# Performance work log

Measured on AMD Instinct MI355X. Metric: run time of the kernel, lower is better.

Reference implementation:

```python
import jax, jax.numpy as jnp
import numpy as np

N, E = 50000, 800000          # nodes, directed edges
DIN, DH, DOUT = 128, 256, 128  # feature dims


def setup_inputs() -> dict:
    key = jax.random.key(0)
    ks = jax.random.split(key, 8)
    glorot = lambda k, fin, fout: jax.random.normal(k, (fin, fout), jnp.float32) * np.float32(1.0 / np.sqrt(fin))
    x = jax.random.normal(ks[0], (N, DIN), jnp.float32)
    edge_index = jax.random.randint(ks[1], (2, E), 0, N, dtype=jnp.int64)
    return {
        "x": x,
        "edge_index": edge_index,
        "W1_l": glorot(ks[2], DIN, DH),   # applied to aggregated neighbors
        "b1": jnp.zeros((DH,), jnp.float32),
        "W1_r": glorot(ks[3], DIN, DH),   # root weight
        "W2_l": glorot(ks[4], DH, DOUT),
        "b2": jnp.zeros((DOUT,), jnp.float32),
        "W2_r": glorot(ks[5], DH, DOUT),
    }


def _sage_conv(x, src, dst, W_l, b, W_r):
    """PyG SAGEConv (mean aggr): lin_l(mean_j x_j) + lin_r(x_i)."""
    n = x.shape[0]
    agg = jax.ops.segment_sum(x[src], dst, num_segments=n)          # [N, D]
    deg = jax.ops.segment_sum(jnp.ones((src.shape[0], 1), x.dtype), dst, num_segments=n)
    agg = agg / jnp.maximum(deg, 1.0)                               # mean over in-neighbors
    return agg @ W_l + b + x @ W_r


def reference(x, edge_index, W1_l, b1, W1_r, W2_l, b2, W2_r):
    src, dst = edge_index[0], edge_index[1]
    h = jax.nn.relu(_sage_conv(x, src, dst, W1_l, b1, W1_r))
    return _sage_conv(h, src, dst, W2_l, b2, W2_r)
```

## Files before the change

kernel.cpp:

```cpp
#include <hip/hip_runtime.h>
#include <hip/hip_bf16.h>
#include <cstdint>


static inline size_t align_up(size_t x, size_t a) { return (x + a - 1) & ~(a - 1); }

using short8 = __attribute__((ext_vector_type(8))) short;
using f32x4  = __attribute__((ext_vector_type(4))) float;

#define BSHIFT 6
#define PB 98

__device__ __forceinline__ float bfpair_lo(unsigned int v) {
  union { unsigned int i; float f; } u; u.i = v << 16; return u.f;
}
__device__ __forceinline__ float bfpair_hi(unsigned int v) {
  union { unsigned int i; float f; } u; u.i = v & 0xffff0000u; return u.f;
}
__device__ __forceinline__ unsigned short f2bf(float f) {
  union { float f; unsigned int i; } u; u.f = f;
  unsigned int r = u.i + 0x7fffu + ((u.i >> 16) & 1u);
  return (unsigned short)(r >> 16);
}

__device__ __forceinline__ void gload_lds16(const void* g, void* l) {
  __builtin_amdgcn_global_load_lds(
      (const __attribute__((address_space(1))) void*)g,
      (__attribute__((address_space(3))) void*)l, 16, 0, 0);
}


__global__ __launch_bounds__(256) void bhist_kernel(const int* __restrict__ dst,
                                                    int* __restrict__ blockhist,
                                                    int E, int chunk) {
  __shared__ int h[1024];
  const int t = threadIdx.x;
  const int pb = blockIdx.x;
  #pragma unroll
  for (int i = t; i < 1024; i += 256) h[i] = 0;
  __syncthreads();
  const int e0 = pb * chunk;
  int e1 = e0 + chunk; if (e1 > E) e1 = E;
  for (int e = e0 + t; e < e1; e += 256) atomicAdd(&h[dst[e] >> BSHIFT], 1);
  __syncthreads();
  #pragma unroll
  for (int i = t; i < 1024; i += 256) blockhist[pb * 1024 + i] = h[i];
}

__global__ __launch_bounds__(1024) void scan_all_kernel(int* __restrict__ blockhist,
                                                        int* __restrict__ brow, int NB) {
  const int i = threadIdx.x;
  int run = 0;
  for (int pb = 0; pb < PB; ++pb) {
    int v = blockhist[pb * 1024 + i];
    blockhist[pb * 1024 + i] = run;
    run += v;
  }
  const int lane = i & 63, w = i >> 6;
  int inc = run;
  #pragma unroll
  for (int off = 1; off < 64; off <<= 1) {
    int u = __shfl_up(inc, off, 64);
    if (lane >= off) inc += u;
  }
  __shared__ int wsum[16];
  if (lane == 63) wsum[w] = inc;
  __syncthreads();
  int woff = 0;
  for (int k = 0; k < w; ++k) woff += wsum[k];
  int excl = woff + inc - run;
  if (i < NB) brow[i] = excl;
  if (i == 1023) brow[NB] = woff + inc;
}

__global__ __launch_bounds__(256) void bin2_kernel(const int* __restrict__ src,
                                                   const int* __restrict__ dst,
                                                   const int* __restrict__ brow,
                                                   const int* __restrict__ blockhist,
                                                   unsigned* __restrict__ stage,
                                                   int E, int NB, int chunk) {
  __shared__ int cur[1024];
  const int t = threadIdx.x;
  const int pb = blockIdx.x;
  for (int i = t; i < 1024; i += 256)
    cur[i] = (i < NB) ? (brow[i] + blockhist[pb * 1024 + i]) : 0;
  __syncthreads();
  const int e0 = pb * chunk;
  int e1 = e0 + chunk; if (e1 > E) e1 = E;
  for (int e = e0 + t; e < e1; e += 256) {
    int d = dst[e];
    int p = atomicAdd(&cur[d >> BSHIFT], 1);
    stage[p] = (unsigned)src[e] | ((unsigned)(d & 63) << 16);
  }
}

__global__ __launch_bounds__(256) void scatter2b_kernel(const unsigned* __restrict__ stage,
                                                        const int* __restrict__ brow,
                                                        int* __restrict__ rowptr,
                                                        unsigned short* __restrict__ col,
                                                        int N, int E) {
  __shared__ int dcnt[64];
  __shared__ int dbase[64];
  const int b = blockIdx.x;
  const int t = threadIdx.x;
  const int n0 = b << BSHIFT;
  const int lo = brow[b], hi = brow[b + 1];
  if (t < 64) dcnt[t] = 0;
  __syncthreads();
  for (int e = lo + t; e < hi; e += 256) atomicAdd(&dcnt[stage[e] >> 16], 1);
  __syncthreads();
  if (t < 64) {
    int v = dcnt[t];
    int inc = v;
    #pragma unroll
    for (int off = 1; off < 64; off <<= 1) {
      int u = __shfl_up(inc, off, 64);
      if (t >= off) inc += u;
    }
    int excl = lo + inc - v;
    dbase[t] = excl;
    dcnt[t] = 0;
    if (n0 + t < N) rowptr[n0 + t] = excl;
  }
  if (b == 0 && t == 0) rowptr[N] = E;
  __syncthreads();
  for (int e = lo + t; e < hi; e += 256) {
    unsigned pr = stage[e];
    int d = pr >> 16;
    int p = atomicAdd(&dcnt[d], 1);
    col[dbase[d] + p] = (unsigned short)(pr & 0xffffu);
  }
}

__global__ __launch_bounds__(256) void prep_kernel(
    const float* __restrict__ x,
    const float* __restrict__ W1l, const float* __restrict__ W1r,
    const float* __restrict__ W2l, const float* __restrict__ W2r,
    __hip_bfloat16* __restrict__ BT1, __hip_bfloat16* __restrict__ BT2,
    __hip_bfloat16* __restrict__ A1, int total4) {
  const int bb = blockIdx.x;
  const int t = threadIdx.x;
  if (bb < 512) {
    int idx = (bb & 255) * 256 + t;
    int n = idx >> 8, k = idx & 255;
    if (bb < 256) {
      float v = (k < 128) ? W1l[k * 256 + n] : W1r[(k - 128) * 256 + n];
      BT1[idx] = __float2bfloat16(v);
    } else {
      float v = (n < 128) ? W2l[k * 128 + n] : W2r[k * 128 + (n - 128)];
      BT2[idx] = __float2bfloat16(v);
    }
    return;
  }
  int idx = (bb - 512) * 256 + t;
  if (idx >= total4) return;
  int i = idx >> 5, j4 = (idx & 31) << 2;
  float4 v = *reinterpret_cast<const float4*>(x + (size_t)i * 128 + j4);
  unsigned p0 = ((unsigned)f2bf(v.y) << 16) | f2bf(v.x);
  unsigned p1 = ((unsigned)f2bf(v.w) << 16) | f2bf(v.z);
  *reinterpret_cast<uint2*>(A1 + (size_t)i * 256 + 128 + j4) = make_uint2(p0, p1);
}


__global__ __launch_bounds__(64) void agg1_kernel(const int* __restrict__ rowptr,
                                                  const unsigned short* __restrict__ col,
                                                  __hip_bfloat16* __restrict__ A1) {
  const int i = blockIdx.x;
  const int t = threadIdx.x;
  const int beg = rowptr[i], end = rowptr[i + 1];
  float ax = 0.f, ay = 0.f;
  int e = beg;
  for (; e + 3 < end; e += 4) {
    int s0 = col[e], s1 = col[e + 1], s2 = col[e + 2], s3 = col[e + 3];
    unsigned v0 = *reinterpret_cast<const unsigned*>(A1 + (size_t)s0 * 256 + 128 + t * 2);
    unsigned v1 = *reinterpret_cast<const unsigned*>(A1 + (size_t)s1 * 256 + 128 + t * 2);
    unsigned v2 = *reinterpret_cast<const unsigned*>(A1 + (size_t)s2 * 256 + 128 + t * 2);
    unsigned v3 = *reinterpret_cast<const unsigned*>(A1 + (size_t)s3 * 256 + 128 + t * 2);
    ax += (bfpair_lo(v0) + bfpair_lo(v1)) + (bfpair_lo(v2) + bfpair_lo(v3));
    ay += (bfpair_hi(v0) + bfpair_hi(v1)) + (bfpair_hi(v2) + bfpair_hi(v3));
  }
  for (; e < end; ++e) {
    int s0 = col[e];
    unsigned v0 = *reinterpret_cast<const unsigned*>(A1 + (size_t)s0 * 256 + 128 + t * 2);
    ax += bfpair_lo(v0);
    ay += bfpair_hi(v0);
  }
  int d = end - beg;
  float inv = 1.0f / (float)(d > 1 ? d : 1);
  unsigned pk = ((unsigned)f2bf(ay * inv) << 16) | f2bf(ax * inv);
  *reinterpret_cast<unsigned*>(A1 + (size_t)i * 256 + t * 2) = pk;
}

__global__ __launch_bounds__(64) void agg2_kernel(const __hip_bfloat16* __restrict__ hw2,
                                                  const int* __restrict__ rowptr,
                                                  const unsigned short* __restrict__ col,
                                                  const float* __restrict__ b2,
                                                  float* __restrict__ out) {
  const int i = blockIdx.x;
  const int t = threadIdx.x;
  const int beg = rowptr[i], end = rowptr[i + 1];
  float ax = 0.f, ay = 0.f;
  int e = beg;
  for (; e + 3 < end; e += 4) {
    int s0 = col[e], s1 = col[e + 1], s2 = col[e + 2], s3 = col[e + 3];
    unsigned v0 = *reinterpret_cast<const unsigned*>(hw2 + (size_t)s0 * 256 + t * 2);
    unsigned v1 = *reinterpret_cast<const unsigned*>(hw2 + (size_t)s1 * 256 + t * 2);
    unsigned v2 = *reinterpret_cast<const unsigned*>(hw2 + (size_t)s2 * 256 + t * 2);
    unsigned v3 = *reinterpret_cast<const unsigned*>(hw2 + (size_t)s3 * 256 + t * 2);
    ax += (bfpair_lo(v0) + bfpair_lo(v1)) + (bfpair_lo(v2) + bfpair_lo(v3));
    ay += (bfpair_hi(v0) + bfpair_hi(v1)) + (bfpair_hi(v2) + bfpair_hi(v3));
  }
  for (; e < end; ++e) {
    int s0 = col[e];
    unsigned v0 = *reinterpret_cast<const unsigned*>(hw2 + (size_t)s0 * 256 + t * 2);
    ax += bfpair_lo(v0);
    ay += bfpair_hi(v0);
  }
  int d = end - beg;
  float inv = 1.0f / (float)(d > 1 ? d : 1);
  unsigned sv = *reinterpret_cast<const unsigned*>(hw2 + (size_t)i * 256 + 128 + t * 2);
  float2 bb = *reinterpret_cast<const float2*>(b2 + t * 2);
  float2 r;
  r.x = ax * inv + bfpair_lo(sv) + bb.x;
  r.y = ay * inv + bfpair_hi(sv) + bb.y;
  *reinterpret_cast<float2*>(out + (size_t)i * 128 + t * 2) = r;
}

__global__ __launch_bounds__(256) void gemm_fused_kernel(
    const __hip_bfloat16* __restrict__ A1,
    const __hip_bfloat16* __restrict__ BT1,
    const __hip_bfloat16* __restrict__ BT2,
    const float* __restrict__ b1,
    __hip_bfloat16* __restrict__ hw2,
    int M) {
  __shared__ __hip_bfloat16 As[64 * 32];
  __shared__ __hip_bfloat16 Bs[256 * 32];
  __shared__ __hip_bfloat16 hLds[64 * 256];
  const int t = threadIdx.x;
  const int lane = t & 63;
  const int w = t >> 6;
  const int wc = w * 64;
  const int bm = blockIdx.x * 64;

  const int srow4 = lane >> 2;
  const int sbyte = (lane & 3) * 16;
  const int fr = lane & 15;
  const int fbyte = (lane >> 4) * 16;
  const int kslot = lane >> 4;

  f32x4 acc[4][4];
  #pragma unroll
  for (int i = 0; i < 4; ++i)
    #pragma unroll
    for (int j = 0; j < 4; ++j) acc[i][j] = (f32x4)(0.f);

  for (int k0 = 0; k0 < 256; k0 += 32) {
    {
      int gr = bm + w * 16 + srow4;
      if (gr >= M) gr = M - 1;
      gload_lds16((const char*)A1 + (size_t)gr * 512 + k0 * 2 + sbyte,
                  (char*)As + w * 1024);
    }
    #pragma unroll
    for (int q = 0; q < 4; ++q) {
      const int c = w * 4 + q;
      const int row = c * 16 + srow4;
      gload_lds16((const char*)BT1 + (size_t)row * 512 + k0 * 2 + sbyte,
                  (char*)Bs + c * 1024);
    }
    __syncthreads();
    short8 af[4], bf[4];
    #pragma unroll
    for (int i = 0; i < 4; ++i) {
      af[i] = *reinterpret_cast<const short8*>((const char*)As + (fr + i * 16) * 64 + fbyte);
      bf[i] = *reinterpret_cast<const short8*>((const char*)Bs + (wc + fr + i * 16) * 64 + fbyte);
    }
    #pragma unroll
    for (int i = 0; i < 4; ++i)
      #pragma unroll
      for (int j = 0; j < 4; ++j)
        acc[i][j] = __builtin_amdgcn_mfma_f32_16x16x32_bf16(af[i], bf[j], acc[i][j], 0, 0, 0);
    __syncthreads();
  }

  {
    const int c0 = wc + fr;
    const int r0 = (lane >> 4) * 4;
    float bj[4];
    #pragma unroll
    for (int j = 0; j < 4; ++j) bj[j] = b1[c0 + j * 16];
    #pragma unroll
    for (int i = 0; i < 4; ++i) {
      #pragma unroll
      for (int j = 0; j < 4; ++j) {
        const int c = c0 + j * 16;
        #pragma unroll
        for (int q = 0; q < 4; ++q) {
          const int r = r0 + i * 16 + q;
          float v = fmaxf(acc[i][j][q] + bj[j], 0.f);
          const int byte = r * 512 + (((c >> 3) ^ (r & 7)) << 4) + ((c & 7) << 1);
          *reinterpret_cast<__hip_bfloat16*>((char*)hLds + byte) = __float2bfloat16(v);
        }
      }
    }
  }

  #pragma unroll
  for (int i = 0; i < 4; ++i)
    #pragma unroll
    for (int j = 0; j < 4; ++j) acc[i][j] = (f32x4)(0.f);

  for (int k0 = 0; k0 < 256; k0 += 32) {
    #pragma unroll
    for (int q = 0; q < 4; ++q) {
      const int c = w * 4 + q;
      const int row = c * 16 + srow4;
      gload_lds16((const char*)BT2 + (size_t)row * 512 + k0 * 2 + sbyte,
                  (char*)Bs + c * 1024);
    }
    __syncthreads();
    short8 af[4], bf[4];
    const int ks = (k0 >> 3) + kslot;
    #pragma unroll
    for (int i = 0; i < 4; ++i) {
      const int ra = fr + i * 16;
      af[i] = *reinterpret_cast<const short8*>(
          (const char*)hLds + ra * 512 + ((ks ^ (ra & 7)) << 4));
      bf[i] = *reinterpret_cast<const short8*>((const char*)Bs + (wc + fr + i * 16) * 64 + fbyte);
    }
    #pragma unroll
    for (int i = 0; i < 4; ++i)
      #pragma unroll
      for (int j = 0; j < 4; ++j)
        acc[i][j] = __builtin_amdgcn_mfma_f32_16x16x32_bf16(af[i], bf[j], acc[i][j], 0, 0, 0);
    __syncthreads();
  }

  {
    const int c0 = wc + fr;
    const int r0 = (lane >> 4) * 4;
    #pragma unroll
    for (int i = 0; i < 4; ++i) {
      #pragma unroll
      for (int q = 0; q < 4; ++q) {
        const int r = bm + r0 + i * 16 + q;
        if (r < M) {
          #pragma unroll
          for (int j = 0; j < 4; ++j)
            hw2[(size_t)r * 256 + c0 + j * 16] = __float2bfloat16(acc[i][j][q]);
        }
      }
    }
  }
}


extern "C" void kernel_launch(void* const* d_in, const int* in_sizes, int n_in,
                              void* d_out, int out_size, void* d_ws, size_t ws_size,
                              hipStream_t stream) {
  const float* x    = (const float*)d_in[0];
  const int*   edge = (const int*)d_in[1];
  const float* W1_l = (const float*)d_in[2];
  const float* b1   = (const float*)d_in[3];
  const float* W1_r = (const float*)d_in[4];
  const float* W2_l = (const float*)d_in[5];
  const float* b2   = (const float*)d_in[6];
  const float* W2_r = (const float*)d_in[7];
  float* out = (float*)d_out;

  const int N = in_sizes[0] / 128;
  const int E = in_sizes[1] / 2;
  const int* srcv = edge;
  const int* dstv = edge + E;
  const int NB = (N + (1 << BSHIFT) - 1) >> BSHIFT;

  char* ws = (char*)d_ws;
  size_t off = 0;
  auto alloc = [&](size_t bytes) -> void* {
    void* p = ws + off;
    off += align_up(bytes, 256);
    return p;
  };
  int* rowptr    = (int*)alloc((size_t)(N + 1) * 4);
  int* brow      = (int*)alloc((size_t)(NB + 1) * 4);
  int* blockhist = (int*)alloc((size_t)PB * 1024 * 4);
  unsigned short* col = (unsigned short*)alloc((size_t)E * 2);
  unsigned* stage = (unsigned*)alloc((size_t)E * 4);
  __hip_bfloat16* BT1 = (__hip_bfloat16*)alloc(256 * 256 * 2);
  __hip_bfloat16* BT2 = (__hip_bfloat16*)alloc(256 * 256 * 2);
  __hip_bfloat16* A1  = (__hip_bfloat16*)alloc((size_t)N * 256 * 2);
  __hip_bfloat16* hw2 = (__hip_bfloat16*)alloc((size_t)N * 256 * 2);

  const int conv_blocks = (N * 32 + 255) / 256;
  prep_kernel<<<512 + conv_blocks, 256, 0, stream>>>(x, W1_l, W1_r, W2_l, W2_r,
                                                     BT1, BT2, A1, N * 32);

  const int chunk = (E + PB - 1) / PB;
  bhist_kernel<<<PB, 256, 0, stream>>>(dstv, blockhist, E, chunk);
  scan_all_kernel<<<1, 1024, 0, stream>>>(blockhist, brow, NB);
  bin2_kernel<<<PB, 256, 0, stream>>>(srcv, dstv, brow, blockhist, stage, E, NB, chunk);
  scatter2b_kernel<<<NB, 256, 0, stream>>>(stage, brow, rowptr, col, N, E);

  agg1_kernel<<<N, 64, 0, stream>>>(rowptr, col, A1);

  gemm_fused_kernel<<<(N + 63) / 64, 256, 0, stream>>>(A1, BT1, BT2, b1, hw2, N);

  agg2_kernel<<<N, 64, 0, stream>>>(hw2, rowptr, col, b2, out);
}
```

Baseline: 159.6 us.

## Fuse CSR build into one persistent kernel with grid barriers; unroll gathers by eight

Merges the histogram, scan, binning and scatter kernels into a single 98-block kernel that separates phases with atomic-counter grid barriers, removing three launches and their gaps. The single-block serial scan over 98 histograms becomes a parallel wave-level scan spread across blocks. The final scatter phase now runs on 98 blocks that each handle eight buckets in turn, instead of one block per bucket. The aggregation gather loops are unrolled to eight edges so more loads are in flight. The barrier relies on all 98 blocks being resident at once, and the barrier counters need a memset before each run.

```diff
diff --git a/kernel.cpp b/kernel.cpp
--- a/kernel.cpp
+++ b/kernel.cpp
@@ -29,106 +29,136 @@
       (__attribute__((address_space(3))) void*)l, 16, 0, 0);
 }
 
-
-__global__ __launch_bounds__(256) void bhist_kernel(const int* __restrict__ dst,
-                                                    int* __restrict__ blockhist,
-                                                    int E, int chunk) {
-  __shared__ int h[1024];
+__device__ __forceinline__ void gbar(int* bar, int nblocks) {
+  __syncthreads();
+  if (threadIdx.x == 0) {
+    __builtin_amdgcn_fence(__ATOMIC_RELEASE, "agent");
+    int prev = __hip_atomic_fetch_add(&bar[0], 1, __ATOMIC_RELAXED,
+                                      __HIP_MEMORY_SCOPE_AGENT);
+    if (prev + 1 == nblocks) {
+      __hip_atomic_store(&bar[1], 1, __ATOMIC_RELAXED, __HIP_MEMORY_SCOPE_AGENT);
+    } else {
+      while (!__hip_atomic_load(&bar[1], __ATOMIC_RELAXED,
+                                __HIP_MEMORY_SCOPE_AGENT))
+        __builtin_amdgcn_s_sleep(2);
+    }
+    __builtin_amdgcn_fence(__ATOMIC_ACQUIRE, "agent");
+  }
+  __syncthreads();
+}
+
+
+__global__ __launch_bounds__(256) void csr_kernel(
+    const int* __restrict__ src, const int* __restrict__ dst,
+    int* __restrict__ blockhist, int* __restrict__ btot,
+    int* __restrict__ brow, unsigned* __restrict__ stage,
+    int* __restrict__ rowptr, unsigned short* __restrict__ col,
+    int* __restrict__ bar, int N, int E, int NB, int chunk) {
+  __shared__ int lds_i[1024];
   const int t = threadIdx.x;
   const int pb = blockIdx.x;
-  #pragma unroll
-  for (int i = t; i < 1024; i += 256) h[i] = 0;
+  const int e0 = pb * chunk;
+  const int e1 = min(e0 + chunk, E);
+
+  for (int i = t; i < 1024; i += 256) lds_i[i] = 0;
   __syncthreads();
-  const int e0 = pb * chunk;
-  int e1 = e0 + chunk; if (e1 > E) e1 = E;
-  for (int e = e0 + t; e < e1; e += 256) atomicAdd(&h[dst[e] >> BSHIFT], 1);
+  for (int e = e0 + t; e < e1; e += 256) atomicAdd(&lds_i[dst[e] >> BSHIFT], 1);
   __syncthreads();
-  #pragma unroll
-  for (int i = t; i < 1024; i += 256) blockhist[pb * 1024 + i] = h[i];
-}
-
-__global__ __launch_bounds__(1024) void scan_all_kernel(int* __restrict__ blockhist,
-                                                        int* __restrict__ brow, int NB) {
-  const int i = threadIdx.x;
-  int run = 0;
-  for (int pb = 0; pb < PB; ++pb) {
-    int v = blockhist[pb * 1024 + i];
-    blockhist[pb * 1024 + i] = run;
-    run += v;
-  }
-  const int lane = i & 63, w = i >> 6;
-  int inc = run;
-  #pragma unroll
-  for (int off = 1; off < 64; off <<= 1) {
-    int u = __shfl_up(inc, off, 64);
-    if (lane >= off) inc += u;
-  }
-  __shared__ int wsum[16];
-  if (lane == 63) wsum[w] = inc;
+  for (int i = t; i < 1024; i += 256) blockhist[pb * 1024 + i] = lds_i[i];
+  gbar(bar + 0, PB);
+
+  {
+    const int lane = t & 63, w = t >> 6;
+    for (int r = 0;; ++r) {
+      const int idx = w + 4 * r;
+      if (idx >= 11) break;
+      const int i = pb + PB * idx;
+      if (i >= 1024) break;
+      int v0 = blockhist[lane * 1024 + i];
+      int v1 = (64 + lane < PB) ? blockhist[(64 + lane) * 1024 + i] : 0;
+      int s0 = v0, s1 = v1;
+      #pragma unroll
+      for (int off = 1; off < 64; off <<= 1) {
+        int u0 = __shfl_up(s0, off, 64);
+        int u1 = __shfl_up(s1, off, 64);
+        if (lane >= off) { s0 += u0; s1 += u1; }
+      }
+      int T0 = __shfl(s0, 63, 64);
+      blockhist[lane * 1024 + i] = s0 - v0;
+      if (64 + lane < PB) blockhist[(64 + lane) * 1024 + i] = T0 + s1 - v1;
+      if (lane == 63) btot[i] = T0 + s1;
+    }
+  }
+  gbar(bar + 2, PB);
+
+  if (pb == 0) {
+    int4 v = *reinterpret_cast<const int4*>(btot + t * 4);
+    int tsum = v.x + v.y + v.z + v.w;
+    const int lane = t & 63, w = t >> 6;
+    int inc = tsum;
+    #pragma unroll
+    for (int off = 1; off < 64; off <<= 1) {
+      int u = __shfl_up(inc, off, 64);
+      if (lane >= off) inc += u;
+    }
+    if (lane == 63) lds_i[w] = inc;
+    __syncthreads();
+    int woff = 0;
+    for (int k = 0; k < w; ++k) woff += lds_i[k];
+    int e0x = woff + inc - tsum;
+    const int base = t * 4;
+    int p0 = e0x, p1 = p0 + v.x, p2 = p1 + v.y, p3 = p2 + v.z;
+    if (base + 0 < NB) brow[base + 0] = p0;
+    if (base + 1 < NB) brow[base + 1] = p1;
+    if (base + 2 < NB) brow[base + 2] = p2;
+    if (base + 3 < NB) brow[base + 3] = p3;
+    __syncthreads();
+    if (t == 0) brow[NB] = lds_i[0] + lds_i[1] + lds_i[2] + lds_i[3];
+  }
+  gbar(bar + 4, PB);
+
+  for (int i = t; i < 1024; i += 256)
+    lds_i[i] = (i < NB) ? (brow[i] + blockhist[pb * 1024 + i]) : 0;
   __syncthreads();
-  int woff = 0;
-  for (int k = 0; k < w; ++k) woff += wsum[k];
-  int excl = woff + inc - run;
-  if (i < NB) brow[i] = excl;
-  if (i == 1023) brow[NB] = woff + inc;
-}
-
-__global__ __launch_bounds__(256) void bin2_kernel(const int* __restrict__ src,
-                                                   const int* __restrict__ dst,
-                                                   const int* __restrict__ brow,
-                                                   const int* __restrict__ blockhist,
-                                                   unsigned* __restrict__ stage,
-                                                   int E, int NB, int chunk) {
-  __shared__ int cur[1024];
-  const int t = threadIdx.x;
-  const int pb = blockIdx.x;
-  for (int i = t; i < 1024; i += 256)
-    cur[i] = (i < NB) ? (brow[i] + blockhist[pb * 1024 + i]) : 0;
-  __syncthreads();
-  const int e0 = pb * chunk;
-  int e1 = e0 + chunk; if (e1 > E) e1 = E;
   for (int e = e0 + t; e < e1; e += 256) {
     int d = dst[e];
-    int p = atomicAdd(&cur[d >> BSHIFT], 1);
+    int p = atomicAdd(&lds_i[d >> BSHIFT], 1);
     stage[p] = (unsigned)src[e] | ((unsigned)(d & 63) << 16);
   }
-}
-
-__global__ __launch_bounds__(256) void scatter2b_kernel(const unsigned* __restrict__ stage,
-                                                        const int* __restrict__ brow,
-                                                        int* __restrict__ rowptr,
-                                                        unsigned short* __restrict__ col,
-                                                        int N, int E) {
-  __shared__ int dcnt[64];
-  __shared__ int dbase[64];
-  const int b = blockIdx.x;
-  const int t = threadIdx.x;
-  const int n0 = b << BSHIFT;
-  const int lo = brow[b], hi = brow[b + 1];
-  if (t < 64) dcnt[t] = 0;
-  __syncthreads();
-  for (int e = lo + t; e < hi; e += 256) atomicAdd(&dcnt[stage[e] >> 16], 1);
-  __syncthreads();
-  if (t < 64) {
-    int v = dcnt[t];
-    int inc = v;
-    #pragma unroll
-    for (int off = 1; off < 64; off <<= 1) {
-      int u = __shfl_up(inc, off, 64);
-      if (t >= off) inc += u;
-    }
-    int excl = lo + inc - v;
-    dbase[t] = excl;
-    dcnt[t] = 0;
-    if (n0 + t < N) rowptr[n0 + t] = excl;
-  }
-  if (b == 0 && t == 0) rowptr[N] = E;
-  __syncthreads();
-  for (int e = lo + t; e < hi; e += 256) {
-    unsigned pr = stage[e];
-    int d = pr >> 16;
-    int p = atomicAdd(&dcnt[d], 1);
-    col[dbase[d] + p] = (unsigned short)(pr & 0xffffu);
+  gbar(bar + 6, PB);
+
+  if (pb == 0 && t == 0) rowptr[N] = E;
+  int* dcnt = lds_i;
+  int* dbase = lds_i + 64;
+  const int bbe = min(pb * 8 + 8, NB);
+  for (int bb = pb * 8; bb < bbe; ++bb) {
+    const int n0 = bb << BSHIFT;
+    const int lo = brow[bb], hi = brow[bb + 1];
+    __syncthreads();
+    if (t < 64) dcnt[t] = 0;
+    __syncthreads();
+    for (int e = lo + t; e < hi; e += 256) atomicAdd(&dcnt[stage[e] >> 16], 1);
+    __syncthreads();
+    if (t < 64) {
+      int v = dcnt[t];
+      int inc = v;
+      #pragma unroll
+      for (int off = 1; off < 64; off <<= 1) {
+        int u = __shfl_up(inc, off, 64);
+        if (t >= off) inc += u;
+      }
+      int excl = lo + inc - v;
+      dbase[t] = excl;
+      dcnt[t] = 0;
+      if (n0 + t < N) rowptr[n0 + t] = excl;
+    }
+    __syncthreads();
+    for (int e = lo + t; e < hi; e += 256) {
+      unsigned pr = stage[e];
+      int d = pr >> 16;
+      int p = atomicAdd(&dcnt[d], 1);
+      col[dbase[d] + p] = (unsigned short)(pr & 0xffffu);
+    }
   }
 }
 
@@ -170,18 +200,28 @@
   const int beg = rowptr[i], end = rowptr[i + 1];
   float ax = 0.f, ay = 0.f;
   int e = beg;
-  for (; e + 3 < end; e += 4) {
-    int s0 = col[e], s1 = col[e + 1], s2 = col[e + 2], s3 = col[e + 3];
-    unsigned v0 = *reinterpret_cast<const unsigned*>(A1 + (size_t)s0 * 256 + 128 + t * 2);
-    unsigned v1 = *reinterpret_cast<const unsigned*>(A1 + (size_t)s1 * 256 + 128 + t * 2);
-    unsigned v2 = *reinterpret_cast<const unsigned*>(A1 + (size_t)s2 * 256 + 128 + t * 2);
-    unsigned v3 = *reinterpret_cast<const unsigned*>(A1 + (size_t)s3 * 256 + 128 + t * 2);
-    ax += (bfpair_lo(v0) + bfpair_lo(v1)) + (bfpair_lo(v2) + bfpair_lo(v3));
-    ay += (bfpair_hi(v0) + bfpair_hi(v1)) + (bfpair_hi(v2) + bfpair_hi(v3));
-  }
-  for (; e < end; ++e) {
-    int s0 = col[e];
-    unsigned v0 = *reinterpret_cast<const unsigned*>(A1 + (size_t)s0 * 256 + 128 + t * 2);
+  for (; e + 7 < end; e += 8) {
+    unsigned v0 = *reinterpret_cast<const unsigned*>(A1 + (size_t)col[e]     * 256 + 128 + t * 2);
+    unsigned v1 = *reinterpret_cast<const unsigned*>(A1 + (size_t)col[e + 1] * 256 + 128 + t * 2);
+    unsigned v2 = *reinterpret_cast<const unsigned*>(A1 + (size_t)col[e + 2] * 256 + 128 + t * 2);
+    unsigned v3 = *reinterpret_cast<const unsigned*>(A1 + (size_t)col[e + 3] * 256 + 128 + t * 2);
+    unsigned v4 = *reinterpret_cast<const unsigned*>(A1 + (size_t)col[e + 4] * 256 + 128 + t * 2);
+    unsigned v5 = *reinterpret_cast<const unsigned*>(A1 + (size_t)col[e + 5] * 256 + 128 + t * 2);
+    unsigned v6 = *reinterpret_cast<const unsigned*>(A1 + (size_t)col[e + 6] * 256 + 128 + t * 2);
+    unsigned v7 = *reinterpret_cast<const unsigned*>(A1 + (size_t)col[e + 7] * 256 + 128 + t * 2);
+    ax += ((bfpair_lo(v0) + bfpair_lo(v1)) + (bfpair_lo(v2) + bfpair_lo(v3))) +
+          ((bfpair_lo(v4) + bfpair_lo(v5)) + (bfpair_lo(v6) + bfpair_lo(v7)));
+    ay += ((bfpair_hi(v0) + bfpair_hi(v1)) + (bfpair_hi(v2) + bfpair_hi(v3))) +
+          ((bfpair_hi(v4) + bfpair_hi(v5)) + (bfpair_hi(v6) + bfpair_hi(v7)));
+  }
+  for (; e + 1 < end; e += 2) {
+    unsigned v0 = *reinterpret_cast<const unsigned*>(A1 + (size_t)col[e]     * 256 + 128 + t * 2);
+    unsigned v1 = *reinterpret_cast<const unsigned*>(A1 + (size_t)col[e + 1] * 256 + 128 + t * 2);
+    ax += bfpair_lo(v0) + bfpair_lo(v1);
+    ay += bfpair_hi(v0) + bfpair_hi(v1);
+  }
+  if (e < end) {
+    unsigned v0 = *reinterpret_cast<const unsigned*>(A1 + (size_t)col[e] * 256 + 128 + t * 2);
     ax += bfpair_lo(v0);
     ay += bfpair_hi(v0);
   }
@@ -201,18 +241,28 @@
   const int beg = rowptr[i], end = rowptr[i + 1];
   float ax = 0.f, ay = 0.f;
   int e = beg;
-  for (; e + 3 < end; e += 4) {
-    int s0 = col[e], s1 = col[e + 1], s2 = col[e + 2], s3 = col[e + 3];
-    unsigned v0 = *reinterpret_cast<const unsigned*>(hw2 + (size_t)s0 * 256 + t * 2);
-    unsigned v1 = *reinterpret_cast<const unsigned*>(hw2 + (size_t)s1 * 256 + t * 2);
-    unsigned v2 = *reinterpret_cast<const unsigned*>(hw2 + (size_t)s2 * 256 + t * 2);
-    unsigned v3 = *reinterpret_cast<const unsigned*>(hw2 + (size_t)s3 * 256 + t * 2);
-    ax += (bfpair_lo(v0) + bfpair_lo(v1)) + (bfpair_lo(v2) + bfpair_lo(v3));
-    ay += (bfpair_hi(v0) + bfpair_hi(v1)) + (bfpair_hi(v2) + bfpair_hi(v3));
-  }
-  for (; e < end; ++e) {
-    int s0 = col[e];
-    unsigned v0 = *reinterpret_cast<const unsigned*>(hw2 + (size_t)s0 * 256 + t * 2);
+  for (; e + 7 < end; e += 8) {
+    unsigned v0 = *reinterpret_cast<const unsigned*>(hw2 + (size_t)col[e]     * 256 + t * 2);
+    unsigned v1 = *reinterpret_cast<const unsigned*>(hw2 + (size_t)col[e + 1] * 256 + t * 2);
+    unsigned v2 = *reinterpret_cast<const unsigned*>(hw2 + (size_t)col[e + 2] * 256 + t * 2);
+    unsigned v3 = *reinterpret_cast<const unsigned*>(hw2 + (size_t)col[e + 3] * 256 + t * 2);
+    unsigned v4 = *reinterpret_cast<const unsigned*>(hw2 + (size_t)col[e + 4] * 256 + t * 2);
+    unsigned v5 = *reinterpret_cast<const unsigned*>(hw2 + (size_t)col[e + 5] * 256 + t * 2);
+    unsigned v6 = *reinterpret_cast<const unsigned*>(hw2 + (size_t)col[e + 6] * 256 + t * 2);
+    unsigned v7 = *reinterpret_cast<const unsigned*>(hw2 + (size_t)col[e + 7] * 256 + t * 2);
+    ax += ((bfpair_lo(v0) + bfpair_lo(v1)) + (bfpair_lo(v2) + bfpair_lo(v3))) +
+          ((bfpair_lo(v4) + bfpair_lo(v5)) + (bfpair_lo(v6) + bfpair_lo(v7)));
+    ay += ((bfpair_hi(v0) + bfpair_hi(v1)) + (bfpair_hi(v2) + bfpair_hi(v3))) +
+          ((bfpair_hi(v4) + bfpair_hi(v5)) + (bfpair_hi(v6) + bfpair_hi(v7)));
+  }
+  for (; e + 1 < end; e += 2) {
+    unsigned v0 = *reinterpret_cast<const unsigned*>(hw2 + (size_t)col[e]     * 256 + t * 2);
+    unsigned v1 = *reinterpret_cast<const unsigned*>(hw2 + (size_t)col[e + 1] * 256 + t * 2);
+    ax += bfpair_lo(v0) + bfpair_lo(v1);
+    ay += bfpair_hi(v0) + bfpair_hi(v1);
+  }
+  if (e < end) {
+    unsigned v0 = *reinterpret_cast<const unsigned*>(hw2 + (size_t)col[e] * 256 + t * 2);
     ax += bfpair_lo(v0);
     ay += bfpair_hi(v0);
   }
@@ -381,8 +431,10 @@
     off += align_up(bytes, 256);
     return p;
   };
+  int* bar       = (int*)alloc(64);
   int* rowptr    = (int*)alloc((size_t)(N + 1) * 4);
   int* brow      = (int*)alloc((size_t)(NB + 1) * 4);
+  int* btot      = (int*)alloc(1024 * 4);
   int* blockhist = (int*)alloc((size_t)PB * 1024 * 4);
   unsigned short* col = (unsigned short*)alloc((size_t)E * 2);
   unsigned* stage = (unsigned*)alloc((size_t)E * 4);
@@ -391,15 +443,15 @@
   __hip_bfloat16* A1  = (__hip_bfloat16*)alloc((size_t)N * 256 * 2);
   __hip_bfloat16* hw2 = (__hip_bfloat16*)alloc((size_t)N * 256 * 2);
 
+  hipMemsetAsync(bar, 0, 64, stream);
+
   const int conv_blocks = (N * 32 + 255) / 256;
   prep_kernel<<<512 + conv_blocks, 256, 0, stream>>>(x, W1_l, W1_r, W2_l, W2_r,
                                                      BT1, BT2, A1, N * 32);
 
   const int chunk = (E + PB - 1) / PB;
-  bhist_kernel<<<PB, 256, 0, stream>>>(dstv, blockhist, E, chunk);
-  scan_all_kernel<<<1, 1024, 0, stream>>>(blockhist, brow, NB);
-  bin2_kernel<<<PB, 256, 0, stream>>>(srcv, dstv, brow, blockhist, stage, E, NB, chunk);
-  scatter2b_kernel<<<NB, 256, 0, stream>>>(stage, brow, rowptr, col, N, E);
+  csr_kernel<<<PB, 256, 0, stream>>>(srcv, dstv, blockhist, btot, brow, stage,
+                                     rowptr, col, bar, N, E, NB, chunk);
 
   agg1_kernel<<<N, 64, 0, stream>>>(rowptr, col, A1);
 
```

After: 191.4 us. 19.9% more time.

## Merge setup kernels, fold block-histogram scan into binning, widen aggregation loads

Applied to the files above, without the earlier changes.

Merges the weight/feature conversion kernel with the per-block destination histogram kernel into one launch. The separate single-block scan kernel goes away: every binning block now redundantly scans all block histograms to find its own offsets, and block 0 writes the bucket row pointers. The two aggregation kernels now have each half-wave handle alternate edges with 8-byte loads, unroll up to 16 edges, and combine the halves with a cross-lane shuffle. The aim is to cut two launches and the serial scan, and to get more memory-level parallelism in the gathers. The cost is redundant histogram reads in every binning block.

```diff
diff --git a/kernel.cpp b/kernel.cpp
--- a/kernel.cpp
+++ b/kernel.cpp
@@ -29,67 +29,112 @@
       (__attribute__((address_space(3))) void*)l, 16, 0, 0);
 }
 
-
-__global__ __launch_bounds__(256) void bhist_kernel(const int* __restrict__ dst,
-                                                    int* __restrict__ blockhist,
-                                                    int E, int chunk) {
+__global__ __launch_bounds__(256) void setup_kernel(
+    const int* __restrict__ dst, int* __restrict__ blockhist, int E, int chunk,
+    const float* __restrict__ x,
+    const float* __restrict__ W1l, const float* __restrict__ W1r,
+    const float* __restrict__ W2l, const float* __restrict__ W2r,
+    __hip_bfloat16* __restrict__ BT1, __hip_bfloat16* __restrict__ BT2,
+    __hip_bfloat16* __restrict__ A1, int total4) {
   __shared__ int h[1024];
+  const int bb = blockIdx.x;
+  const int t = threadIdx.x;
+  if (bb < PB) {
+    #pragma unroll
+    for (int i = t; i < 1024; i += 256) h[i] = 0;
+    __syncthreads();
+    const int e0 = bb * chunk;
+    int e1 = e0 + chunk; if (e1 > E) e1 = E;
+    for (int e = e0 + t; e < e1; e += 256) atomicAdd(&h[dst[e] >> BSHIFT], 1);
+    __syncthreads();
+    #pragma unroll
+    for (int i = t; i < 1024; i += 256) blockhist[bb * 1024 + i] = h[i];
+    return;
+  }
+  const int wb = bb - PB;
+  if (wb < 512) {
+    int idx = (wb & 255) * 256 + t;
+    int n = idx >> 8, k = idx & 255;
+    if (wb < 256) {
+      float v = (k < 128) ? W1l[k * 256 + n] : W1r[(k - 128) * 256 + n];
+      BT1[idx] = __float2bfloat16(v);
+    } else {
+      float v = (n < 128) ? W2l[k * 128 + n] : W2r[k * 128 + (n - 128)];
+      BT2[idx] = __float2bfloat16(v);
+    }
+    return;
+  }
+  int idx = (wb - 512) * 256 + t;
+  if (idx >= total4) return;
+  int i = idx >> 5, j4 = (idx & 31) << 2;
+  float4 v = *reinterpret_cast<const float4*>(x + (size_t)i * 128 + j4);
+  unsigned p0 = ((unsigned)f2bf(v.y) << 16) | f2bf(v.x);
+  unsigned p1 = ((unsigned)f2bf(v.w) << 16) | f2bf(v.z);
+  *reinterpret_cast<uint2*>(A1 + (size_t)i * 256 + 128 + j4) = make_uint2(p0, p1);
+}
+
+__global__ __launch_bounds__(256) void bin2_kernel(const int* __restrict__ src,
+                                                   const int* __restrict__ dst,
+                                                   const int* __restrict__ blockhist,
+                                                   unsigned* __restrict__ stage,
+                                                   int* __restrict__ brow,
+                                                   int E, int NB, int chunk) {
+  __shared__ int tot_lds[1024];
+  __shared__ int cur_lds[1024];
+  __shared__ int wsum[4];
   const int t = threadIdx.x;
   const int pb = blockIdx.x;
+
+  int run[4] = {0, 0, 0, 0};
+  int ownp[4] = {0, 0, 0, 0};
+  for (int pb2 = 0; pb2 < PB; ++pb2) {
+    #pragma unroll
+    for (int j = 0; j < 4; ++j) {
+      int v = blockhist[pb2 * 1024 + t + 256 * j];
+      if (pb2 == pb) ownp[j] = run[j];
+      run[j] += v;
+    }
+  }
   #pragma unroll
-  for (int i = t; i < 1024; i += 256) h[i] = 0;
-  __syncthreads();
-  const int e0 = pb * chunk;
-  int e1 = e0 + chunk; if (e1 > E) e1 = E;
-  for (int e = e0 + t; e < e1; e += 256) atomicAdd(&h[dst[e] >> BSHIFT], 1);
-  __syncthreads();
-  #pragma unroll
-  for (int i = t; i < 1024; i += 256) blockhist[pb * 1024 + i] = h[i];
-}
-
-__global__ __launch_bounds__(1024) void scan_all_kernel(int* __restrict__ blockhist,
-                                                        int* __restrict__ brow, int NB) {
-  const int i = threadIdx.x;
-  int run = 0;
-  for (int pb = 0; pb < PB; ++pb) {
-    int v = blockhist[pb * 1024 + i];
-    blockhist[pb * 1024 + i] = run;
-    run += v;
-  }
-  const int lane = i & 63, w = i >> 6;
-  int inc = run;
+  for (int j = 0; j < 4; ++j) {
+    tot_lds[t + 256 * j] = run[j];
+    cur_lds[t + 256 * j] = ownp[j];
+  }
+  __syncthreads();
+
+  int4 v = *reinterpret_cast<const int4*>(&tot_lds[t * 4]);
+  int tsum = v.x + v.y + v.z + v.w;
+  const int lane = t & 63, w = t >> 6;
+  int inc = tsum;
   #pragma unroll
   for (int off = 1; off < 64; off <<= 1) {
     int u = __shfl_up(inc, off, 64);
     if (lane >= off) inc += u;
   }
-  __shared__ int wsum[16];
   if (lane == 63) wsum[w] = inc;
   __syncthreads();
   int woff = 0;
   for (int k = 0; k < w; ++k) woff += wsum[k];
-  int excl = woff + inc - run;
-  if (i < NB) brow[i] = excl;
-  if (i == 1023) brow[NB] = woff + inc;
-}
-
-__global__ __launch_bounds__(256) void bin2_kernel(const int* __restrict__ src,
-                                                   const int* __restrict__ dst,
-                                                   const int* __restrict__ brow,
-                                                   const int* __restrict__ blockhist,
-                                                   unsigned* __restrict__ stage,
-                                                   int E, int NB, int chunk) {
-  __shared__ int cur[1024];
-  const int t = threadIdx.x;
-  const int pb = blockIdx.x;
-  for (int i = t; i < 1024; i += 256)
-    cur[i] = (i < NB) ? (brow[i] + blockhist[pb * 1024 + i]) : 0;
-  __syncthreads();
+  int e0x = woff + inc - tsum;
+  int p0 = e0x, p1 = p0 + v.x, p2 = p1 + v.y, p3 = p2 + v.z;
+  cur_lds[t * 4 + 0] += p0;
+  cur_lds[t * 4 + 1] += p1;
+  cur_lds[t * 4 + 2] += p2;
+  cur_lds[t * 4 + 3] += p3;
+  if (pb == 0) {
+    if (t * 4 + 0 < NB) brow[t * 4 + 0] = p0;
+    if (t * 4 + 1 < NB) brow[t * 4 + 1] = p1;
+    if (t * 4 + 2 < NB) brow[t * 4 + 2] = p2;
+    if (t * 4 + 3 < NB) brow[t * 4 + 3] = p3;
+    if (t == 255) brow[NB] = p3 + v.w;
+  }
+  __syncthreads();
+
   const int e0 = pb * chunk;
-  int e1 = e0 + chunk; if (e1 > E) e1 = E;
+  const int e1 = min(e0 + chunk, E);
   for (int e = e0 + t; e < e1; e += 256) {
     int d = dst[e];
-    int p = atomicAdd(&cur[d >> BSHIFT], 1);
+    int p = atomicAdd(&cur_lds[d >> BSHIFT], 1);
     stage[p] = (unsigned)src[e] | ((unsigned)(d & 63) << 16);
   }
 }
@@ -132,63 +177,68 @@
   }
 }
 
-__global__ __launch_bounds__(256) void prep_kernel(
-    const float* __restrict__ x,
-    const float* __restrict__ W1l, const float* __restrict__ W1r,
-    const float* __restrict__ W2l, const float* __restrict__ W2r,
-    __hip_bfloat16* __restrict__ BT1, __hip_bfloat16* __restrict__ BT2,
-    __hip_bfloat16* __restrict__ A1, int total4) {
-  const int bb = blockIdx.x;
-  const int t = threadIdx.x;
-  if (bb < 512) {
-    int idx = (bb & 255) * 256 + t;
-    int n = idx >> 8, k = idx & 255;
-    if (bb < 256) {
-      float v = (k < 128) ? W1l[k * 256 + n] : W1r[(k - 128) * 256 + n];
-      BT1[idx] = __float2bfloat16(v);
-    } else {
-      float v = (n < 128) ? W2l[k * 128 + n] : W2r[k * 128 + (n - 128)];
-      BT2[idx] = __float2bfloat16(v);
-    }
-    return;
-  }
-  int idx = (bb - 512) * 256 + t;
-  if (idx >= total4) return;
-  int i = idx >> 5, j4 = (idx & 31) << 2;
-  float4 v = *reinterpret_cast<const float4*>(x + (size_t)i * 128 + j4);
-  unsigned p0 = ((unsigned)f2bf(v.y) << 16) | f2bf(v.x);
-  unsigned p1 = ((unsigned)f2bf(v.w) << 16) | f2bf(v.z);
-  *reinterpret_cast<uint2*>(A1 + (size_t)i * 256 + 128 + j4) = make_uint2(p0, p1);
-}
-
+
+#define AGG_LOAD(TBL, OFFS)                                                    \
+  {                                                                            \
+    int s = col[eidx];                                                         \
+    uint2 vv = *reinterpret_cast<const uint2*>(TBL + (size_t)s * 256 + OFFS + q * 4); \
+    a0 += bfpair_lo(vv.x); a1 += bfpair_hi(vv.x);                              \
+    a2 += bfpair_lo(vv.y); a3 += bfpair_hi(vv.y);                              \
+  }
 
 __global__ __launch_bounds__(64) void agg1_kernel(const int* __restrict__ rowptr,
                                                   const unsigned short* __restrict__ col,
                                                   __hip_bfloat16* __restrict__ A1) {
   const int i = blockIdx.x;
   const int t = threadIdx.x;
+  const int half = t >> 5;
+  const int q = t & 31;
   const int beg = rowptr[i], end = rowptr[i + 1];
-  float ax = 0.f, ay = 0.f;
+  float a0 = 0.f, a1 = 0.f, a2 = 0.f, a3 = 0.f;
   int e = beg;
-  for (; e + 3 < end; e += 4) {
-    int s0 = col[e], s1 = col[e + 1], s2 = col[e + 2], s3 = col[e + 3];
-    unsigned v0 = *reinterpret_cast<const unsigned*>(A1 + (size_t)s0 * 256 + 128 + t * 2);
-    unsigned v1 = *reinterpret_cast<const unsigned*>(A1 + (size_t)s1 * 256 + 128 + t * 2);
-    unsigned v2 = *reinterpret_cast<const unsigned*>(A1 + (size_t)s2 * 256 + 128 + t * 2);
-    unsigned v3 = *reinterpret_cast<const unsigned*>(A1 + (size_t)s3 * 256 + 128 + t * 2);
-    ax += (bfpair_lo(v0) + bfpair_lo(v1)) + (bfpair_lo(v2) + bfpair_lo(v3));
-    ay += (bfpair_hi(v0) + bfpair_hi(v1)) + (bfpair_hi(v2) + bfpair_hi(v3));
-  }
-  for (; e < end; ++e) {
-    int s0 = col[e];
-    unsigned v0 = *reinterpret_cast<const unsigned*>(A1 + (size_t)s0 * 256 + 128 + t * 2);
-    ax += bfpair_lo(v0);
-    ay += bfpair_hi(v0);
-  }
-  int d = end - beg;
-  float inv = 1.0f / (float)(d > 1 ? d : 1);
-  unsigned pk = ((unsigned)f2bf(ay * inv) << 16) | f2bf(ax * inv);
-  *reinterpret_cast<unsigned*>(A1 + (size_t)i * 256 + t * 2) = pk;
+  for (; e + 15 < end; e += 16) {
+    #pragma unroll
+    for (int u = 0; u < 8; ++u) {
+      int eidx = e + 2 * u + half;
+      AGG_LOAD(A1, 128)
+    }
+  }
+  if (e + 7 < end) {
+    #pragma unroll
+    for (int u = 0; u < 4; ++u) {
+      int eidx = e + 2 * u + half;
+      AGG_LOAD(A1, 128)
+    }
+    e += 8;
+  }
+  if (e + 3 < end) {
+    #pragma unroll
+    for (int u = 0; u < 2; ++u) {
+      int eidx = e + 2 * u + half;
+      AGG_LOAD(A1, 128)
+    }
+    e += 4;
+  }
+  if (e + 1 < end) {
+    int eidx = e + half;
+    AGG_LOAD(A1, 128)
+    e += 2;
+  }
+  if (e < end && half == 0) {
+    int eidx = e;
+    AGG_LOAD(A1, 128)
+  }
+  a0 += __shfl_xor(a0, 32, 64);
+  a1 += __shfl_xor(a1, 32, 64);
+  a2 += __shfl_xor(a2, 32, 64);
+  a3 += __shfl_xor(a3, 32, 64);
+  const int d = end - beg;
+  const float inv = 1.0f / (float)(d > 1 ? d : 1);
+  if (half == 0) {
+    unsigned p0 = ((unsigned)f2bf(a1 * inv) << 16) | f2bf(a0 * inv);
+    unsigned p1 = ((unsigned)f2bf(a3 * inv) << 16) | f2bf(a2 * inv);
+    *reinterpret_cast<uint2*>(A1 + (size_t)i * 256 + q * 4) = make_uint2(p0, p1);
+  }
 }
 
 __global__ __launch_bounds__(64) void agg2_kernel(const __hip_bfloat16* __restrict__ hw2,
@@ -198,32 +248,59 @@
                                                   float* __restrict__ out) {
   const int i = blockIdx.x;
   const int t = threadIdx.x;
+  const int half = t >> 5;
+  const int q = t & 31;
   const int beg = rowptr[i], end = rowptr[i + 1];
-  float ax = 0.f, ay = 0.f;
+  float a0 = 0.f, a1 = 0.f, a2 = 0.f, a3 = 0.f;
   int e = beg;
-  for (; e + 3 < end; e += 4) {
-    int s0 = col[e], s1 = col[e + 1], s2 = col[e + 2], s3 = col[e + 3];
-    unsigned v0 = *reinterpret_cast<const unsigned*>(hw2 + (size_t)s0 * 256 + t * 2);
-    unsigned v1 = *reinterpret_cast<const unsigned*>(hw2 + (size_t)s1 * 256 + t * 2);
-    unsigned v2 = *reinterpret_cast<const unsigned*>(hw2 + (size_t)s2 * 256 + t * 2);
-    unsigned v3 = *reinterpret_cast<const unsigned*>(hw2 + (size_t)s3 * 256 + t * 2);
-    ax += (bfpair_lo(v0) + bfpair_lo(v1)) + (bfpair_lo(v2) + bfpair_lo(v3));
-    ay += (bfpair_hi(v0) + bfpair_hi(v1)) + (bfpair_hi(v2) + bfpair_hi(v3));
-  }
-  for (; e < end; ++e) {
-    int s0 = col[e];
-    unsigned v0 = *reinterpret_cast<const unsigned*>(hw2 + (size_t)s0 * 256 + t * 2);
-    ax += bfpair_lo(v0);
-    ay += bfpair_hi(v0);
-  }
-  int d = end - beg;
-  float inv = 1.0f / (float)(d > 1 ? d : 1);
-  unsigned sv = *reinterpret_cast<const unsigned*>(hw2 + (size_t)i * 256 + 128 + t * 2);
-  float2 bb = *reinterpret_cast<const float2*>(b2 + t * 2);
-  float2 r;
-  r.x = ax * inv + bfpair_lo(sv) + bb.x;
-  r.y = ay * inv + bfpair_hi(sv) + bb.y;
-  *reinterpret_cast<float2*>(out + (size_t)i * 128 + t * 2) = r;
+  for (; e + 15 < end; e += 16) {
+    #pragma unroll
+    for (int u = 0; u < 8; ++u) {
+      int eidx = e + 2 * u + half;
+      AGG_LOAD(hw2, 0)
+    }
+  }
+  if (e + 7 < end) {
+    #pragma unroll
+    for (int u = 0; u < 4; ++u) {
+      int eidx = e + 2 * u + half;
+      AGG_LOAD(hw2, 0)
+    }
+    e += 8;
+  }
+  if (e + 3 < end) {
+    #pragma unroll
+    for (int u = 0; u < 2; ++u) {
+      int eidx = e + 2 * u + half;
+      AGG_LOAD(hw2, 0)
+    }
+    e += 4;
+  }
+  if (e + 1 < end) {
+    int eidx = e + half;
+    AGG_LOAD(hw2, 0)
+    e += 2;
+  }
+  if (e < end && half == 0) {
+    int eidx = e;
+    AGG_LOAD(hw2, 0)
+  }
+  a0 += __shfl_xor(a0, 32, 64);
+  a1 += __shfl_xor(a1, 32, 64);
+  a2 += __shfl_xor(a2, 32, 64);
+  a3 += __shfl_xor(a3, 32, 64);
+  const int d = end - beg;
+  const float inv = 1.0f / (float)(d > 1 ? d : 1);
+  if (half == 0) {
+    uint2 sv = *reinterpret_cast<const uint2*>(hw2 + (size_t)i * 256 + 128 + q * 4);
+    float4 bb = *reinterpret_cast<const float4*>(b2 + q * 4);
+    float4 r;
+    r.x = a0 * inv + bfpair_lo(sv.x) + bb.x;
+    r.y = a1 * inv + bfpair_hi(sv.x) + bb.y;
+    r.z = a2 * inv + bfpair_lo(sv.y) + bb.z;
+    r.w = a3 * inv + bfpair_hi(sv.y) + bb.w;
+    *reinterpret_cast<float4*>(out + (size_t)i * 128 + q * 4) = r;
+  }
 }
 
 __global__ __launch_bounds__(256) void gemm_fused_kernel(
@@ -391,14 +468,12 @@
   __hip_bfloat16* A1  = (__hip_bfloat16*)alloc((size_t)N * 256 * 2);
   __hip_bfloat16* hw2 = (__hip_bfloat16*)alloc((size_t)N * 256 * 2);
 
+  const int chunk = (E + PB - 1) / PB;
   const int conv_blocks = (N * 32 + 255) / 256;
-  prep_kernel<<<512 + conv_blocks, 256, 0, stream>>>(x, W1_l, W1_r, W2_l, W2_r,
-                                                     BT1, BT2, A1, N * 32);
-
-  const int chunk = (E + PB - 1) / PB;
-  bhist_kernel<<<PB, 256, 0, stream>>>(dstv, blockhist, E, chunk);
-  scan_all_kernel<<<1, 1024, 0, stream>>>(blockhist, brow, NB);
-  bin2_kernel<<<PB, 256, 0, stream>>>(srcv, dstv, brow, blockhist, stage, E, NB, chunk);
+  setup_kernel<<<PB + 512 + conv_blocks, 256, 0, stream>>>(
+      dstv, blockhist, E, chunk, x, W1_l, W1_r, W2_l, W2_r, BT1, BT2, A1, N * 32);
+
+  bin2_kernel<<<PB, 256, 0, stream>>>(srcv, dstv, blockhist, stage, brow, E, NB, chunk);
   scatter2b_kernel<<<NB, 256, 0, stream>>>(stage, brow, rowptr, col, N, E);
 
   agg1_kernel<<<N, 64, 0, stream>>>(rowptr, col, A1);
```

Measured after the change: 152.0 us. 4.8% less time.
